# Kernel tuning notes

Measured on AMD Instinct MI355X. Metric: run time of the kernel, lower is better.

## Reference

```python
import jax, jax.numpy as jnp
import numpy as np

N = 100000
D = 512


def setup_inputs() -> dict:
    key = jax.random.key(0)
    k1, k2 = jax.random.split(key)
    features = jax.random.normal(k1, (N, D), dtype=jnp.float32)
    attn_w = jax.random.normal(k2, (D,), dtype=jnp.float32)
    attn_b = jnp.zeros((1,), dtype=jnp.float32)
    return {"features": features, "attn_w": attn_w, "attn_b": attn_b, "k": 4}


def reference(features, attn_w, attn_b, k):
    # features: [N, D]; sliding-window (half-width k, truncated at edges) mean
    n = features.shape[0]
    zero = jnp.zeros((1, features.shape[1]), dtype=features.dtype)
    cs = jnp.concatenate([zero, jnp.cumsum(features, axis=0)], axis=0)  # [N+1, D]
    i = jnp.arange(n)
    lo = jnp.maximum(i - k, 0)          # inclusive window start
    hi = jnp.minimum(i + k, n - 1)      # inclusive window end
    win_sum = cs[hi + 1] - cs[lo]       # [N, D]
    count = (hi - lo + 1).astype(features.dtype)[:, None]
    agg = win_sum / count               # [N, D] windowed means
    scores = agg @ attn_w + attn_b[0]   # [N]
    w = jax.nn.softmax(scores, axis=0)  # [N]
    bag = w @ agg                       # [D]
    return bag, w
```

## Files before the change

kernel.cpp:

```cpp
#include <hip/hip_runtime.h>
#include <math.h>

#define D 512
#define NB_P 1000

__global__ void k_dot(const float* __restrict__ f, const float* __restrict__ w,
                      float* __restrict__ dot, int n) {
    int wave = threadIdx.x >> 6;
    int lane = threadIdx.x & 63;
    int row  = blockIdx.x * 4 + wave;
    if (row >= n) return;
    const float4* fr = (const float4*)(f + (size_t)row * D);
    const float4* wr = (const float4*)w;
    float4 a0 = fr[lane],      b0 = wr[lane];
    float4 a1 = fr[lane + 64], b1 = wr[lane + 64];
    float s = a0.x*b0.x + a0.y*b0.y + a0.z*b0.z + a0.w*b0.w
            + a1.x*b1.x + a1.y*b1.y + a1.z*b1.z + a1.w*b1.w;
    #pragma unroll
    for (int off = 32; off; off >>= 1) s += __shfl_down(s, off);
    if (lane == 0) dot[row] = s;
}

__global__ void k_eu(const float* __restrict__ dot, const float* __restrict__ bptr,
                     const int* __restrict__ kptr, float* __restrict__ e_out,
                     float* __restrict__ uu, float* __restrict__ psum, int n) {
    int j = blockIdx.x * 256 + threadIdx.x;
    float e_loc = 0.f;
    if (j < n) {
        int k = *kptr;
        float bias = bptr[0];
        int ilo = max(j - k, 0), ihi = min(j + k, n - 1);
        float ut = 0.f;
        for (int i = ilo; i <= ihi; ++i) {
            int lo = max(i - k, 0), hi = min(i + k, n - 1);
            float s = 0.f;
            for (int q = lo; q <= hi; ++q) s += dot[q];
            float cnt = (float)(hi - lo + 1);
            float ei = __expf(s / cnt + bias);
            if (i == j) e_loc = ei;
            ut += ei * __builtin_amdgcn_rcpf(cnt);
        }
        e_out[j] = e_loc;
        uu[j] = ut;
    }
    float e = e_loc;
    #pragma unroll
    for (int off = 32; off; off >>= 1) e += __shfl_down(e, off);
    __shared__ float sm[4];
    int lane = threadIdx.x & 63, wid = threadIdx.x >> 6;
    if (lane == 0) sm[wid] = e;
    __syncthreads();
    if (threadIdx.x == 0)
        psum[blockIdx.x] = sm[0] + sm[1] + sm[2] + sm[3];
}

__global__ void k_pbag(const float* __restrict__ f, const float* __restrict__ u,
                       float* __restrict__ partial, int n, int chunk) {
    int t = threadIdx.x;
    int j0 = blockIdx.x * chunk;
    int j1 = min(j0 + chunk, n);
    float4 acc0 = make_float4(0.f,0.f,0.f,0.f);
    float4 acc1 = make_float4(0.f,0.f,0.f,0.f);
    float4 acc2 = make_float4(0.f,0.f,0.f,0.f);
    float4 acc3 = make_float4(0.f,0.f,0.f,0.f);
    int j = j0;
    for (; j + 4 <= j1; j += 4) {
        float u0 = u[j], u1 = u[j+1], u2 = u[j+2], u3 = u[j+3];
        float4 v0 = ((const float4*)(f + (size_t)(j  ) * D))[t];
        float4 v1 = ((const float4*)(f + (size_t)(j+1) * D))[t];
        float4 v2 = ((const float4*)(f + (size_t)(j+2) * D))[t];
        float4 v3 = ((const float4*)(f + (size_t)(j+3) * D))[t];
        acc0.x += u0*v0.x; acc0.y += u0*v0.y; acc0.z += u0*v0.z; acc0.w += u0*v0.w;
        acc1.x += u1*v1.x; acc1.y += u1*v1.y; acc1.z += u1*v1.z; acc1.w += u1*v1.w;
        acc2.x += u2*v2.x; acc2.y += u2*v2.y; acc2.z += u2*v2.z; acc2.w += u2*v2.w;
        acc3.x += u3*v3.x; acc3.y += u3*v3.y; acc3.z += u3*v3.z; acc3.w += u3*v3.w;
    }
    for (; j < j1; ++j) {
        float uj = u[j];
        float4 v = ((const float4*)(f + (size_t)j * D))[t];
        acc0.x += uj*v.x; acc0.y += uj*v.y; acc0.z += uj*v.z; acc0.w += uj*v.w;
    }
    float4 a;
    a.x = (acc0.x + acc1.x) + (acc2.x + acc3.x);
    a.y = (acc0.y + acc1.y) + (acc2.y + acc3.y);
    a.z = (acc0.z + acc1.z) + (acc2.z + acc3.z);
    a.w = (acc0.w + acc1.w) + (acc2.w + acc3.w);
    ((float4*)(partial + (size_t)blockIdx.x * D))[t] = a;
}

__global__ void k_final(const float* __restrict__ partial, const float* __restrict__ psum,
                        int nbp, int nbs, const float* __restrict__ e,
                        float* __restrict__ bag, float* __restrict__ w_out, int n) {
    __shared__ float sm[4];
    __shared__ float ginv;
    int lane = threadIdx.x & 63, wid = threadIdx.x >> 6;

    float s = 0.f;
    for (int idx = threadIdx.x; idx < nbs; idx += 256) s += psum[idx];
    #pragma unroll
    for (int off = 32; off; off >>= 1) s += __shfl_down(s, off);
    if (lane == 0) sm[wid] = s;
    __syncthreads();
    if (threadIdx.x == 0)
        ginv = 1.f / (sm[0] + sm[1] + sm[2] + sm[3]);
    __syncthreads();
    float inv = ginv;

    if (blockIdx.x < 32) {
        int c = blockIdx.x * 16 + (threadIdx.x & 15);
        int r = threadIdx.x >> 4;
        float acc = 0.f;
        for (int b = r; b < nbp; b += 16) acc += partial[(size_t)b * D + c];
        __shared__ float sred[256];
        sred[threadIdx.x] = acc;
        __syncthreads();
        if (threadIdx.x < 16) {
            float t = 0.f;
            #pragma unroll
            for (int q = 0; q < 16; ++q) t += sred[q * 16 + threadIdx.x];
            bag[blockIdx.x * 16 + threadIdx.x] = t * inv;
        }
    }

    for (int j = blockIdx.x * 256 + threadIdx.x; j < n; j += gridDim.x * 256)
        w_out[j] = e[j] * inv;
}

extern "C" void kernel_launch(void* const* d_in, const int* in_sizes, int n_in,
                              void* d_out, int out_size, void* d_ws, size_t ws_size,
                              hipStream_t stream) {
    const float* f  = (const float*)d_in[0];
    const float* aw = (const float*)d_in[1];
    const float* ab = (const float*)d_in[2];
    const int*   kp = (const int*)d_in[3];
    int n = in_sizes[0] / D;

    float* bag   = (float*)d_out;
    float* w_out = (float*)d_out + D;

    int nb2 = (n + 255) / 256;

    float* wsf     = (float*)d_ws;
    float* dot     = wsf;
    float* e       = wsf + n;
    float* uu      = wsf + 2 * (size_t)n;
    float* psum    = wsf + 3 * (size_t)n;
    size_t poff    = ((3 * (size_t)n + (size_t)nb2) + 31) & ~(size_t)31;
    float* partial = wsf + poff;

    int chunk = (n + NB_P - 1) / NB_P;

    k_dot  <<<(n + 3) / 4, 256, 0, stream>>>(f, aw, dot, n);
    k_eu   <<<nb2, 256, 0, stream>>>(dot, ab, kp, e, uu, psum, n);
    k_pbag <<<NB_P, 128, 0, stream>>>(f, uu, partial, n, chunk);
    k_final<<<nb2, 256, 0, stream>>>(partial, psum, NB_P, nb2, e, bag, w_out, n);
}
```

Measured before the change: 91.82 us.

## Fuse row dot-product and window exp/weight kernels with shared-memory halo tiles

Merges the per-row dot-product kernel and the windowed exp/weight kernel into one kernel. Each block computes dots for 128 owned rows plus an 8-row halo on each side into shared memory, then computes exp values and window-weighted sums from LDS. This drops one launch and the global dot array round trip, and stops recomputing each window's exps redundantly. In exchange about 12% of feature rows are read twice for the halo, and the code assumes k ≤ 8.

```diff
diff --git a/kernel.cpp b/kernel.cpp
--- a/kernel.cpp
+++ b/kernel.cpp
@@ -3,55 +3,78 @@
 
 #define D 512
 #define NB_P 1000
+#define OWN 128
+#define HALOA 8
 
-__global__ void k_dot(const float* __restrict__ f, const float* __restrict__ w,
-                      float* __restrict__ dot, int n) {
-    int wave = threadIdx.x >> 6;
-    int lane = threadIdx.x & 63;
-    int row  = blockIdx.x * 4 + wave;
-    if (row >= n) return;
-    const float4* fr = (const float4*)(f + (size_t)row * D);
-    const float4* wr = (const float4*)w;
-    float4 a0 = fr[lane],      b0 = wr[lane];
-    float4 a1 = fr[lane + 64], b1 = wr[lane + 64];
-    float s = a0.x*b0.x + a0.y*b0.y + a0.z*b0.z + a0.w*b0.w
-            + a1.x*b1.x + a1.y*b1.y + a1.z*b1.z + a1.w*b1.w;
-    #pragma unroll
-    for (int off = 32; off; off >>= 1) s += __shfl_down(s, off);
-    if (lane == 0) dot[row] = s;
+__device__ __forceinline__ float dot4(float4 a, float4 b) {
+    return a.x*b.x + a.y*b.y + a.z*b.z + a.w*b.w;
 }
 
-__global__ void k_eu(const float* __restrict__ dot, const float* __restrict__ bptr,
-                     const int* __restrict__ kptr, float* __restrict__ e_out,
-                     float* __restrict__ uu, float* __restrict__ psum, int n) {
-    int j = blockIdx.x * 256 + threadIdx.x;
-    float e_loc = 0.f;
-    if (j < n) {
-        int k = *kptr;
-        float bias = bptr[0];
-        int ilo = max(j - k, 0), ihi = min(j + k, n - 1);
-        float ut = 0.f;
-        for (int i = ilo; i <= ihi; ++i) {
+__global__ __launch_bounds__(256) void k_a(
+    const float* __restrict__ f, const float* __restrict__ w,
+    const float* __restrict__ bptr, const int* __restrict__ kptr,
+    float* __restrict__ e_out, float* __restrict__ uu,
+    float* __restrict__ psum, int n)
+{
+    __shared__ float dots[OWN + 2 * HALOA];
+    __shared__ float e_sh[OWN + 2 * HALOA];
+    __shared__ float sm[4];
+    int lane = threadIdx.x & 63;
+    int wid  = threadIdx.x >> 6;
+    int t    = threadIdx.x;
+    int g0   = blockIdx.x * OWN - HALOA;
+
+    const float4* wr = (const float4*)w;
+    float4 b0 = wr[lane], b1 = wr[lane + 64];
+
+    for (int lr = wid; lr < OWN + 2 * HALOA; lr += 4) {
+        int row = g0 + lr;
+        bool v = (row >= 0) && (row < n);
+        const float4* fr = (const float4*)(f + (size_t)(v ? row : 0) * D);
+        float4 a0 = fr[lane], a1 = fr[lane + 64];
+        float s = dot4(a0, b0) + dot4(a1, b1);
+        #pragma unroll
+        for (int off = 32; off; off >>= 1) s += __shfl_down(s, off);
+        if (lane == 0) dots[lr] = v ? s : 0.f;
+    }
+    __syncthreads();
+
+    int k = *kptr;
+    float bias = bptr[0];
+
+    float e_reg = 0.f;
+    if (t < OWN + 2 * HALOA) {
+        int i = g0 + t;
+        if (t >= HALOA - k && t < HALOA + OWN + k && i >= 0 && i < n) {
             int lo = max(i - k, 0), hi = min(i + k, n - 1);
             float s = 0.f;
-            for (int q = lo; q <= hi; ++q) s += dot[q];
-            float cnt = (float)(hi - lo + 1);
-            float ei = __expf(s / cnt + bias);
-            if (i == j) e_loc = ei;
-            ut += ei * __builtin_amdgcn_rcpf(cnt);
+            for (int q = lo; q <= hi; ++q) s += dots[q - g0];
+            e_reg = __expf(s / (float)(hi - lo + 1) + bias);
         }
-        e_out[j] = e_loc;
-        uu[j] = ut;
+        e_sh[t] = e_reg;
     }
-    float e = e_loc;
+    __syncthreads();
+
+    float pv = (t >= HALOA && t < HALOA + OWN) ? e_reg : 0.f;
     #pragma unroll
-    for (int off = 32; off; off >>= 1) e += __shfl_down(e, off);
-    __shared__ float sm[4];
-    int lane = threadIdx.x & 63, wid = threadIdx.x >> 6;
-    if (lane == 0) sm[wid] = e;
+    for (int off = 32; off; off >>= 1) pv += __shfl_down(pv, off);
+    if (lane == 0) sm[wid] = pv;
     __syncthreads();
-    if (threadIdx.x == 0)
-        psum[blockIdx.x] = sm[0] + sm[1] + sm[2] + sm[3];
+    if (t == 0) psum[blockIdx.x] = sm[0] + sm[1] + sm[2] + sm[3];
+
+    if (t < OWN) {
+        int j = blockIdx.x * OWN + t;
+        if (j < n) {
+            e_out[j] = e_sh[t + HALOA];
+            int lo = max(j - k, 0), hi = min(j + k, n - 1);
+            float acc = 0.f;
+            for (int i = lo; i <= hi; ++i) {
+                int li = max(i - k, 0), hh = min(i + k, n - 1);
+                acc += e_sh[i - g0] * __builtin_amdgcn_rcpf((float)(hh - li + 1));
+            }
+            uu[j] = acc;
+        }
+    }
 }
 
 __global__ void k_pbag(const float* __restrict__ f, const float* __restrict__ u,
@@ -115,10 +138,10 @@
         sred[threadIdx.x] = acc;
         __syncthreads();
         if (threadIdx.x < 16) {
-            float t = 0.f;
+            float tt = 0.f;
             #pragma unroll
-            for (int q = 0; q < 16; ++q) t += sred[q * 16 + threadIdx.x];
-            bag[blockIdx.x * 16 + threadIdx.x] = t * inv;
+            for (int q = 0; q < 16; ++q) tt += sred[q * 16 + threadIdx.x];
+            bag[blockIdx.x * 16 + threadIdx.x] = tt * inv;
         }
     }
 
@@ -138,20 +161,19 @@
     float* bag   = (float*)d_out;
     float* w_out = (float*)d_out + D;
 
+    int nbA = (n + OWN - 1) / OWN;
     int nb2 = (n + 255) / 256;
 
     float* wsf     = (float*)d_ws;
-    float* dot     = wsf;
-    float* e       = wsf + n;
-    float* uu      = wsf + 2 * (size_t)n;
-    float* psum    = wsf + 3 * (size_t)n;
-    size_t poff    = ((3 * (size_t)n + (size_t)nb2) + 31) & ~(size_t)31;
+    float* e       = wsf;
+    float* uu      = wsf + n;
+    float* psum    = wsf + 2 * (size_t)n;
+    size_t poff    = ((2 * (size_t)n + (size_t)nbA) + 31) & ~(size_t)31;
     float* partial = wsf + poff;
 
     int chunk = (n + NB_P - 1) / NB_P;
 
-    k_dot  <<<(n + 3) / 4, 256, 0, stream>>>(f, aw, dot, n);
-    k_eu   <<<nb2, 256, 0, stream>>>(dot, ab, kp, e, uu, psum, n);
+    k_a    <<<nbA, 256, 0, stream>>>(f, aw, ab, kp, e, uu, psum, n);
     k_pbag <<<NB_P, 128, 0, stream>>>(f, uu, partial, n, chunk);
-    k_final<<<nb2, 256, 0, stream>>>(partial, psum, NB_P, nb2, e, bag, w_out, n);
+    k_final<<<nb2, 256, 0, stream>>>(partial, psum, NB_P, nbA, e, bag, w_out, n);
 }
```

Result: faster. 89.47 us (-2.6%).
